# Kernel tuning notes

Measured on AMD Instinct MI355X. Metric: run time of the kernel, lower is better.

The kernel has to match this reference:

```python
import jax, jax.numpy as jnp
import numpy as np
import math

DIM = 2048
NUM_HEADS = 16
NUM_KV_HEADS = 4
HEAD_DIM = DIM // NUM_HEADS  # 128
KV_DIM = DIM * NUM_KV_HEADS // NUM_HEADS  # 512
B, T = 4, 2048


def setup_inputs() -> dict:
    key = jax.random.key(0)
    ks = jax.random.split(key, 12)
    s = 0.02
    return {
        "x": jax.random.normal(ks[0], (B, T, DIM), dtype=jnp.float32),
        "cos": jax.random.uniform(ks[1], (T, HEAD_DIM // 2), dtype=jnp.float32),
        "sin": jax.random.uniform(ks[2], (T, HEAD_DIM // 2), dtype=jnp.float32),
        "Wq": jax.random.normal(ks[3], (DIM, DIM), dtype=jnp.float32) * s,
        "bq": jnp.zeros((DIM,), dtype=jnp.float32),
        "Wk": jax.random.normal(ks[4], (DIM, KV_DIM), dtype=jnp.float32) * s,
        "bk": jnp.zeros((KV_DIM,), dtype=jnp.float32),
        "Wv": jax.random.normal(ks[5], (DIM, KV_DIM), dtype=jnp.float32) * s,
        "bv": jnp.zeros((KV_DIM,), dtype=jnp.float32),
        "Wo": jax.random.normal(ks[6], (DIM, DIM), dtype=jnp.float32) * s,
        "bo": jnp.zeros((DIM,), dtype=jnp.float32),
    }


def _rope(t, cos, sin):
    # t: [B, H, T, D]; cos/sin: [T, D/2] broadcast over (B, H)
    t1, t2 = t[..., ::2], t[..., 1::2]
    return jnp.concatenate([t1 * cos - t2 * sin, t1 * sin + t2 * cos], axis=-1)


def reference(x, cos, sin, Wq, bq, Wk, bk, Wv, bv, Wo, bo):
    Bx, Tx, C = x.shape
    q = (x @ Wq + bq).reshape(Bx, Tx, NUM_HEADS, HEAD_DIM).transpose(0, 2, 1, 3)
    k = (x @ Wk + bk).reshape(Bx, Tx, NUM_KV_HEADS, HEAD_DIM).transpose(0, 2, 1, 3)
    v = (x @ Wv + bv).reshape(Bx, Tx, NUM_KV_HEADS, HEAD_DIM).transpose(0, 2, 1, 3)
    rep = NUM_HEADS // NUM_KV_HEADS
    k = jnp.repeat(k, rep, axis=1)
    v = jnp.repeat(v, rep, axis=1)
    q = _rope(q, cos, sin)
    k = _rope(k, cos, sin)
    scores = jnp.einsum("bhqd,bhkd->bhqk", q, k) / math.sqrt(HEAD_DIM)
    attn = jax.nn.softmax(scores, axis=-1)
    out = jnp.einsum("bhqk,bhkd->bhqd", attn, v)
    out = out.transpose(0, 2, 1, 3).reshape(Bx, Tx, C)
    return out @ Wo + bo
```

## Files before the change

kernel.cpp:

```cpp
#include <hip/hip_runtime.h>

typedef unsigned short u16;
using bf16x8 = __attribute__((ext_vector_type(8))) short;
using u16x8  = __attribute__((ext_vector_type(8))) unsigned short;
using f32x4  = __attribute__((ext_vector_type(4))) float;
using u32x2  = __attribute__((ext_vector_type(2))) unsigned int;

__device__ __forceinline__ u16 f2bf(float f) {
  unsigned u = __float_as_uint(f);
  u += 0x7FFFu + ((u >> 16) & 1u);
  return (u16)(u >> 16);
}

__device__ __forceinline__ unsigned cvt_pk_bf16(float lo, float hi) {
  unsigned r;
  asm("v_cvt_pk_bf16_f32 %0, %1, %2" : "=v"(r) : "v"(lo), "v"(hi));
  return r;
}

__device__ __forceinline__ void gload_lds16(const void* g, void* l) {
  __builtin_amdgcn_global_load_lds(
      (const __attribute__((address_space(1))) unsigned int*)g,
      (__attribute__((address_space(3))) unsigned int*)l, 16, 0, 0);
}

__global__ __launch_bounds__(256) void k_cvt(const float* __restrict__ src,
                                             u16* __restrict__ dst) {
  size_t i = (size_t)blockIdx.x * 256 + threadIdx.x;
  const float4* s4 = (const float4*)src;
  float4 a = s4[i * 2], b = s4[i * 2 + 1];
  u16x8 r;
  r[0] = f2bf(a.x); r[1] = f2bf(a.y); r[2] = f2bf(a.z); r[3] = f2bf(a.w);
  r[4] = f2bf(b.x); r[5] = f2bf(b.y); r[6] = f2bf(b.z); r[7] = f2bf(b.w);
  *(u16x8*)(dst + i * 8) = r;
}

__global__ void k_transpose_cvt(const float* __restrict__ src, u16* __restrict__ dst,
                                int R, int C) {
  __shared__ float tile[32][33];
  int bx = blockIdx.x * 32, by = blockIdx.y * 32;
  int tx = threadIdx.x, ty = threadIdx.y;
#pragma unroll
  for (int j = 0; j < 4; ++j)
    tile[ty + j * 8][tx] = src[(size_t)(by + ty + j * 8) * C + bx + tx];
  __syncthreads();
#pragma unroll
  for (int j = 0; j < 4; ++j)
    dst[(size_t)(bx + ty + j * 8) * R + by + tx] = f2bf(tile[tx][ty + j * 8]);
}

__device__ __forceinline__ void gemm_core128(const u16* __restrict__ A,
                                             const u16* __restrict__ Bt, int K,
                                             int m0, int n0, u16* As, u16* Bs,
                                             f32x4 acc[4][4]) {
  const int tid  = threadIdx.x;
  const int lane = tid & 63;
  const int w    = tid >> 6;
  const int wr   = (w >> 1) * 64;
  const int wc   = (w & 1) * 64;
  const int srow = (w << 3) + (lane >> 3);
  const int lm   = lane & 15;
  const int lg   = lane >> 4;

  for (int kt = 0; kt < K; kt += 64) {
#pragma unroll
    for (int i = 0; i < 4; ++i) {
      int r  = (i << 5) + srow;
      int cc = (lane & 7) ^ (r & 7);
      gload_lds16(A  + (size_t)(m0 + r) * K + kt + (cc << 3), As + ((i * 4 + w) << 9));
      gload_lds16(Bt + (size_t)(n0 + r) * K + kt + (cc << 3), Bs + ((i * 4 + w) << 9));
    }
    __syncthreads();
#pragma unroll
    for (int kk = 0; kk < 2; ++kk) {
      bf16x8 af[4], bfr[4];
#pragma unroll
      for (int m = 0; m < 4; ++m) {
        const int row = wr + m * 16 + lm;
        af[m] = *(const bf16x8*)(As + row * 64 + ((((kk << 2) + lg) ^ (row & 7)) << 3));
      }
#pragma unroll
      for (int n = 0; n < 4; ++n) {
        const int row = wc + n * 16 + lm;
        bfr[n] = *(const bf16x8*)(Bs + row * 64 + ((((kk << 2) + lg) ^ (row & 7)) << 3));
      }
#pragma unroll
      for (int m = 0; m < 4; ++m)
#pragma unroll
        for (int n = 0; n < 4; ++n)
          acc[m][n] = __builtin_amdgcn_mfma_f32_16x16x32_bf16(af[m], bfr[n], acc[m][n], 0, 0, 0);
    }
    __syncthreads();
  }
}

__global__ __launch_bounds__(256, 2) void k_qkv(
    const u16* __restrict__ xb, const u16* __restrict__ wT,
    const float* __restrict__ bq, const float* __restrict__ bk, const float* __restrict__ bv,
    const float* __restrict__ cosb, const float* __restrict__ sinb,
    u16* __restrict__ qbuf, u16* __restrict__ kbuf, u16* __restrict__ vbufT) {
  __shared__ u16 As[128 * 64], Bs[128 * 64];
  const int mt = blockIdx.x, nt = blockIdx.y;
  f32x4 acc[4][4];
#pragma unroll
  for (int m = 0; m < 4; ++m)
#pragma unroll
    for (int n = 0; n < 4; ++n) { f32x4 z = {0.f, 0.f, 0.f, 0.f}; acc[m][n] = z; }
  gemm_core128(xb, wT, 2048, mt * 128, nt * 128, As, Bs, acc);

  const int lane = threadIdx.x & 63, w = threadIdx.x >> 6;
  const int row0 = mt * 128 + (w >> 1) * 64 + ((lane >> 4) << 2);
  const int col0 = nt * 128 + (w & 1) * 64 + (lane & 15);
  const float qscale = 0.12751744f;

#pragma unroll
  for (int m = 0; m < 4; ++m) {
#pragma unroll
    for (int n = 0; n < 4; ++n) {
      const int gc = col0 + n * 16;
#pragma unroll
      for (int i = 0; i < 4; ++i) {
        const int gr = row0 + m * 16 + i;
        const int b = gr >> 11, t = gr & 2047;
        float v = acc[m][n][i];
        if (nt < 16) {
          int h = gc >> 7, d = gc & 127;
          float val = v + bq[gc];
          float part = __shfl_xor(val, 1);
          int ir = d >> 1;
          float c = cosb[t * 64 + ir], s = sinb[t * 64 + ir];
          float outv; int dd;
          if (d & 1) { outv = part * s + val * c; dd = ir + 64; }
          else       { outv = val * c - part * s; dd = ir; }
          qbuf[(((size_t)(b * 16 + h) * 2048 + t) << 7) + dd] = f2bf(outv * qscale);
        } else if (nt < 20) {
          int g2 = gc - 2048;
          int kvh = g2 >> 7, d = g2 & 127;
          float val = v + bk[g2];
          float part = __shfl_xor(val, 1);
          int ir = d >> 1;
          float c = cosb[t * 64 + ir], s = sinb[t * 64 + ir];
          float outv; int dd;
          if (d & 1) { outv = part * s + val * c; dd = ir + 64; }
          else       { outv = val * c - part * s; dd = ir; }
          kbuf[(((size_t)(b * 4 + kvh) * 2048 + t) << 7) + dd] = f2bf(outv);
        } else {
          int g2 = gc - 2560;
          int kvh = g2 >> 7, d = g2 & 127;
          float val = v + bv[g2];
          vbufT[((size_t)((b * 4 + kvh) * 128 + d)) * 2048 + t] = f2bf(val);
        }
      }
    }
  }
}

__global__ __launch_bounds__(256, 2) void k_attn(const u16* __restrict__ qbuf,
                                                 const u16* __restrict__ kbuf,
                                                 const u16* __restrict__ vbufT,
                                                 u16* __restrict__ ob) {
  __shared__ u16 Ks[2][64 * 128];
  __shared__ u16 Vs[2][128 * 64];
  __shared__ u16 Ps[128 * 64];

  const int f = blockIdx.x;
  const int x = f & 7, mm = f >> 3;
  const int g = x * 2 + (mm >> 6);
  const int mem = mm & 63;
  const int b = g >> 2, kvh = g & 3;
  const int h = kvh * 4 + (mem >> 4);
  const int qt = mem & 15;

  const int tid = threadIdx.x, lane = tid & 63, w = tid >> 6;
  const int lm = lane & 15, lg = lane >> 4;

  const u16* qb = qbuf + ((size_t)((b * 16 + h) * 2048 + qt * 128)) * 128;
  const u16* kb = kbuf + ((size_t)(b * 4 + kvh) * 2048) * 128;
  const u16* vb = vbufT + ((size_t)(b * 4 + kvh) * 128) * 2048;

  bf16x8 qf[2][4];
#pragma unroll
  for (int st = 0; st < 2; ++st)
#pragma unroll
    for (int dc = 0; dc < 4; ++dc)
      qf[st][dc] = *(const bf16x8*)(qb + (size_t)(w * 32 + st * 16 + lm) * 128 + dc * 32 + (lg << 3));

  f32x4 o[2][8];
#pragma unroll
  for (int st = 0; st < 2; ++st)
#pragma unroll
    for (int dn = 0; dn < 8; ++dn) { f32x4 z = {0.f, 0.f, 0.f, 0.f}; o[st][dn] = z; }
  float lsum[2] = {0.f, 0.f};

  auto stage = [&](int buf, int kt) {
#pragma unroll
    for (int j = 0; j < 4; ++j) {
      int s  = w * 4 + j;
      int cK = s * 64 + lane;
      int rK = cK >> 4, ccK = cK & 15;
      gload_lds16(kb + (size_t)(kt + rK) * 128 + ((ccK ^ (rK & 7)) << 3), &Ks[buf][s << 9]);
      int dV = s * 8 + (lane >> 3), ccV = lane & 7;
      gload_lds16(vb + (size_t)dV * 2048 + kt + ((ccV ^ (dV & 7)) << 3), &Vs[buf][s << 9]);
    }
  };

  stage(0, 0);
  int cur = 0;
  for (int t = 0; t < 32; ++t) {
    const int kt = t << 6;
    if (t < 31) {
      stage(cur ^ 1, kt + 64);
      asm volatile("s_waitcnt vmcnt(8)" ::: "memory");
    } else {
      asm volatile("s_waitcnt vmcnt(0)" ::: "memory");
    }
    __builtin_amdgcn_s_barrier();
    __builtin_amdgcn_sched_barrier(0);
    const u16* KsC = Ks[cur];
    const u16* VsC = Vs[cur];

#pragma unroll
    for (int kg = 0; kg < 4; ++kg) {
      const int krow = kg * 16 + lm;
      bf16x8 kf[4];
#pragma unroll
      for (int dc = 0; dc < 4; ++dc)
        kf[dc] = *(const bf16x8*)(KsC + krow * 128 + (((dc * 4 + lg) ^ (krow & 7)) << 3));
      f32x4 s0 = {0.f, 0.f, 0.f, 0.f}, s1 = {0.f, 0.f, 0.f, 0.f};
      __builtin_amdgcn_s_setprio(1);
#pragma unroll
      for (int dc = 0; dc < 4; ++dc) {
        s0 = __builtin_amdgcn_mfma_f32_16x16x32_bf16(kf[dc], qf[0][dc], s0, 0, 0, 0);
        s1 = __builtin_amdgcn_mfma_f32_16x16x32_bf16(kf[dc], qf[1][dc], s1, 0, 0, 0);
      }
      __builtin_amdgcn_s_setprio(0);
#pragma unroll
      for (int st = 0; st < 2; ++st) {
        f32x4 sv = st ? s1 : s0;
        float p0 = __builtin_amdgcn_exp2f(sv[0]);
        float p1 = __builtin_amdgcn_exp2f(sv[1]);
        float p2 = __builtin_amdgcn_exp2f(sv[2]);
        float p3 = __builtin_amdgcn_exp2f(sv[3]);
        lsum[st] += (p0 + p1) + (p2 + p3);
        u32x2 pk;
        pk[0] = cvt_pk_bf16(p0, p1);
        pk[1] = cvt_pk_bf16(p2, p3);
        const int q = w * 32 + st * 16 + lm;
        const int chunk = kg * 2 + (lg >> 1);
        u16* dst = Ps + q * 64 + ((chunk ^ (q & 7)) << 3) + ((lg & 1) << 2);
        *reinterpret_cast<u32x2*>(dst) = pk;
      }
    }

#pragma unroll
    for (int kstep = 0; kstep < 2; ++kstep) {
      bf16x8 pf[2];
#pragma unroll
      for (int st = 0; st < 2; ++st) {
        const int q = w * 32 + st * 16 + lm;
        pf[st] = *(const bf16x8*)(Ps + q * 64 + (((kstep * 4 + lg) ^ (q & 7)) << 3));
      }
      __builtin_amdgcn_s_setprio(1);
#pragma unroll
      for (int dn = 0; dn < 8; ++dn) {
        const int d = dn * 16 + lm;
        bf16x8 vf = *(const bf16x8*)(VsC + d * 64 + (((kstep * 4 + lg) ^ (d & 7)) << 3));
        o[0][dn] = __builtin_amdgcn_mfma_f32_16x16x32_bf16(pf[0], vf, o[0][dn], 0, 0, 0);
        o[1][dn] = __builtin_amdgcn_mfma_f32_16x16x32_bf16(pf[1], vf, o[1][dn], 0, 0, 0);
      }
      __builtin_amdgcn_s_setprio(0);
    }
    __builtin_amdgcn_sched_barrier(0);
    __builtin_amdgcn_s_barrier();
    cur ^= 1;
  }

#pragma unroll
  for (int st = 0; st < 2; ++st) {
    float L = lsum[st];
    L += __shfl_xor(L, 16);
    L += __shfl_xor(L, 32);
#pragma unroll
    for (int i = 0; i < 4; ++i) {
      float inv = 1.0f / __shfl(L, lg * 4 + i);
      int t = qt * 128 + w * 32 + st * 16 + lg * 4 + i;
#pragma unroll
      for (int dn = 0; dn < 8; ++dn) {
        int d = dn * 16 + lm;
        ob[((size_t)(b * 2048 + t)) * 2048 + h * 128 + d] = f2bf(o[st][dn][i] * inv);
      }
    }
  }
}

__global__ __launch_bounds__(256, 2) void k_oproj(const u16* __restrict__ ab,
                                                  const u16* __restrict__ woT,
                                                  const float* __restrict__ bo,
                                                  float* __restrict__ out) {
  __shared__ u16 As[128 * 64], Bs[128 * 64];
  const int mt = blockIdx.x, nt = blockIdx.y;
  f32x4 acc[4][4];
#pragma unroll
  for (int m = 0; m < 4; ++m)
#pragma unroll
    for (int n = 0; n < 4; ++n) { f32x4 z = {0.f, 0.f, 0.f, 0.f}; acc[m][n] = z; }
  gemm_core128(ab, woT, 2048, mt * 128, nt * 128, As, Bs, acc);

  const int lane = threadIdx.x & 63, w = threadIdx.x >> 6;
  const int row0 = mt * 128 + (w >> 1) * 64 + ((lane >> 4) << 2);
  const int col0 = nt * 128 + (w & 1) * 64 + (lane & 15);
#pragma unroll
  for (int m = 0; m < 4; ++m)
#pragma unroll
    for (int n = 0; n < 4; ++n) {
      const int gc = col0 + n * 16;
      const float bias = bo[gc];
#pragma unroll
      for (int i = 0; i < 4; ++i) {
        const int gr = row0 + m * 16 + i;
        out[(size_t)gr * 2048 + gc] = acc[m][n][i] + bias;
      }
    }
}

extern "C" void kernel_launch(void* const* d_in, const int* in_sizes, int n_in,
                              void* d_out, int out_size, void* d_ws, size_t ws_size,
                              hipStream_t stream) {
  const float* x    = (const float*)d_in[0];
  const float* cosb = (const float*)d_in[1];
  const float* sinb = (const float*)d_in[2];
  const float* Wq   = (const float*)d_in[3];
  const float* bq   = (const float*)d_in[4];
  const float* Wk   = (const float*)d_in[5];
  const float* bk   = (const float*)d_in[6];
  const float* Wv   = (const float*)d_in[7];
  const float* bv   = (const float*)d_in[8];
  const float* Wo   = (const float*)d_in[9];
  const float* bo   = (const float*)d_in[10];
  float* out = (float*)d_out;

  u16* ws    = (u16*)d_ws;
  u16* xb    = ws;
  u16* wqkvT = xb    + (size_t)8192 * 2048;
  u16* woT   = wqkvT + (size_t)3072 * 2048;
  u16* qbuf  = woT   + (size_t)2048 * 2048;
  u16* kbuf  = qbuf  + (size_t)8192 * 2048;
  u16* vbufT = kbuf  + (size_t)8192 * 512;
  u16* attn  = xb;

  k_cvt<<<8192, 256, 0, stream>>>(x, xb);
  dim3 tb(32, 8);
  k_transpose_cvt<<<dim3(64, 64), tb, 0, stream>>>(Wq, wqkvT, 2048, 2048);
  k_transpose_cvt<<<dim3(16, 64), tb, 0, stream>>>(Wk, wqkvT + (size_t)2048 * 2048, 2048, 512);
  k_transpose_cvt<<<dim3(16, 64), tb, 0, stream>>>(Wv, wqkvT + (size_t)2560 * 2048, 2048, 512);
  k_transpose_cvt<<<dim3(64, 64), tb, 0, stream>>>(Wo, woT, 2048, 2048);

  k_qkv<<<dim3(64, 24), 256, 0, stream>>>(xb, wqkvT, bq, bk, bv, cosb, sinb, qbuf, kbuf, vbufT);
  k_attn<<<1024, 256, 0, stream>>>(qbuf, kbuf, vbufT, attn);
  k_oproj<<<dim3(64, 16), 256, 0, stream>>>(attn, woT, bo, out);
}
```

Baseline: 374.1 us.

## Use 32x32x16 MFMA in attention and keep P in registers via permlane swap

Rewrites the attention inner loop to use 32x32x16 bf16 MFMAs instead of 16x16x32. The S^T output layout is rearranged with v_permlane32_swap so the exponentiated probabilities feed the PV MFMA directly as A operands. This removes the LDS round trip through the Ps buffer and reduces MFMA instruction count and LDS traffic. In exchange it needs larger accumulator register tiles, which may raise register pressure and hurt occupancy, and it relies on exact lane-layout correctness.

Result: no change. 368.5 us (-1.5%).

```diff
diff --git a/kernel.cpp b/kernel.cpp
--- a/kernel.cpp
+++ b/kernel.cpp
@@ -4,7 +4,8 @@
 using bf16x8 = __attribute__((ext_vector_type(8))) short;
 using u16x8  = __attribute__((ext_vector_type(8))) unsigned short;
 using f32x4  = __attribute__((ext_vector_type(4))) float;
-using u32x2  = __attribute__((ext_vector_type(2))) unsigned int;
+using f32x16 = __attribute__((ext_vector_type(16))) float;
+using u32x4  = __attribute__((ext_vector_type(4))) unsigned int;
 
 __device__ __forceinline__ u16 f2bf(float f) {
   unsigned u = __float_as_uint(f);
@@ -16,6 +17,10 @@
   unsigned r;
   asm("v_cvt_pk_bf16_f32 %0, %1, %2" : "=v"(r) : "v"(lo), "v"(hi));
   return r;
+}
+
+__device__ __forceinline__ void permswap(unsigned& a, unsigned& b) {
+  asm volatile("v_permlane32_swap_b32 %0, %1" : "+v"(a), "+v"(b));
 }
 
 __device__ __forceinline__ void gload_lds16(const void* g, void* l) {
@@ -161,7 +166,6 @@
                                                  u16* __restrict__ ob) {
   __shared__ u16 Ks[2][64 * 128];
   __shared__ u16 Vs[2][128 * 64];
-  __shared__ u16 Ps[128 * 64];
 
   const int f = blockIdx.x;
   const int x = f & 7, mm = f >> 3;
@@ -172,25 +176,24 @@
   const int qt = mem & 15;
 
   const int tid = threadIdx.x, lane = tid & 63, w = tid >> 6;
-  const int lm = lane & 15, lg = lane >> 4;
+  const int l31 = lane & 31, hi = lane >> 5;
 
   const u16* qb = qbuf + ((size_t)((b * 16 + h) * 2048 + qt * 128)) * 128;
   const u16* kb = kbuf + ((size_t)(b * 4 + kvh) * 2048) * 128;
   const u16* vb = vbufT + ((size_t)(b * 4 + kvh) * 128) * 2048;
 
-  bf16x8 qf[2][4];
-#pragma unroll
-  for (int st = 0; st < 2; ++st)
-#pragma unroll
-    for (int dc = 0; dc < 4; ++dc)
-      qf[st][dc] = *(const bf16x8*)(qb + (size_t)(w * 32 + st * 16 + lm) * 128 + dc * 32 + (lg << 3));
-
-  f32x4 o[2][8];
-#pragma unroll
-  for (int st = 0; st < 2; ++st)
-#pragma unroll
-    for (int dn = 0; dn < 8; ++dn) { f32x4 z = {0.f, 0.f, 0.f, 0.f}; o[st][dn] = z; }
-  float lsum[2] = {0.f, 0.f};
+  const int q = w * 32 + l31;
+  bf16x8 qfr[8];
+#pragma unroll
+  for (int kc = 0; kc < 8; ++kc)
+    qfr[kc] = *(const bf16x8*)(qb + (size_t)q * 128 + kc * 16 + hi * 8);
+
+  f32x16 o[4];
+#pragma unroll
+  for (int dt = 0; dt < 4; ++dt)
+#pragma unroll
+    for (int r = 0; r < 16; ++r) o[dt][r] = 0.f;
+  float lsum = 0.f;
 
   auto stage = [&](int buf, int kt) {
 #pragma unroll
@@ -205,90 +208,83 @@
   };
 
   stage(0, 0);
-  int cur = 0;
   for (int t = 0; t < 32; ++t) {
-    const int kt = t << 6;
     if (t < 31) {
-      stage(cur ^ 1, kt + 64);
+      stage((t + 1) & 1, (t + 1) << 6);
       asm volatile("s_waitcnt vmcnt(8)" ::: "memory");
     } else {
       asm volatile("s_waitcnt vmcnt(0)" ::: "memory");
     }
     __builtin_amdgcn_s_barrier();
     __builtin_amdgcn_sched_barrier(0);
-    const u16* KsC = Ks[cur];
-    const u16* VsC = Vs[cur];
-
-#pragma unroll
-    for (int kg = 0; kg < 4; ++kg) {
-      const int krow = kg * 16 + lm;
-      bf16x8 kf[4];
-#pragma unroll
-      for (int dc = 0; dc < 4; ++dc)
-        kf[dc] = *(const bf16x8*)(KsC + krow * 128 + (((dc * 4 + lg) ^ (krow & 7)) << 3));
-      f32x4 s0 = {0.f, 0.f, 0.f, 0.f}, s1 = {0.f, 0.f, 0.f, 0.f};
+    const u16* KsC = Ks[t & 1];
+    const u16* VsC = Vs[t & 1];
+
+    u32x4 pa[4];
+
+#pragma unroll
+    for (int kb2 = 0; kb2 < 2; ++kb2) {
+      const int key = kb2 * 32 + l31;
+      bf16x8 kf[8];
+#pragma unroll
+      for (int kc = 0; kc < 8; ++kc)
+        kf[kc] = *(const bf16x8*)(KsC + key * 128 + (((kc * 2 + hi) ^ (key & 7)) << 3));
+      f32x16 s;
+#pragma unroll
+      for (int r = 0; r < 16; ++r) s[r] = 0.f;
       __builtin_amdgcn_s_setprio(1);
 #pragma unroll
-      for (int dc = 0; dc < 4; ++dc) {
-        s0 = __builtin_amdgcn_mfma_f32_16x16x32_bf16(kf[dc], qf[0][dc], s0, 0, 0, 0);
-        s1 = __builtin_amdgcn_mfma_f32_16x16x32_bf16(kf[dc], qf[1][dc], s1, 0, 0, 0);
-      }
+      for (int kc = 0; kc < 8; ++kc)
+        s = __builtin_amdgcn_mfma_f32_32x32x16_bf16(kf[kc], qfr[kc], s, 0, 0, 0);
       __builtin_amdgcn_s_setprio(0);
-#pragma unroll
-      for (int st = 0; st < 2; ++st) {
-        f32x4 sv = st ? s1 : s0;
-        float p0 = __builtin_amdgcn_exp2f(sv[0]);
-        float p1 = __builtin_amdgcn_exp2f(sv[1]);
-        float p2 = __builtin_amdgcn_exp2f(sv[2]);
-        float p3 = __builtin_amdgcn_exp2f(sv[3]);
-        lsum[st] += (p0 + p1) + (p2 + p3);
-        u32x2 pk;
-        pk[0] = cvt_pk_bf16(p0, p1);
-        pk[1] = cvt_pk_bf16(p2, p3);
-        const int q = w * 32 + st * 16 + lm;
-        const int chunk = kg * 2 + (lg >> 1);
-        u16* dst = Ps + q * 64 + ((chunk ^ (q & 7)) << 3) + ((lg & 1) << 2);
-        *reinterpret_cast<u32x2*>(dst) = pk;
-      }
-    }
-
-#pragma unroll
-    for (int kstep = 0; kstep < 2; ++kstep) {
-      bf16x8 pf[2];
-#pragma unroll
-      for (int st = 0; st < 2; ++st) {
-        const int q = w * 32 + st * 16 + lm;
-        pf[st] = *(const bf16x8*)(Ps + q * 64 + (((kstep * 4 + lg) ^ (q & 7)) << 3));
-      }
-      __builtin_amdgcn_s_setprio(1);
-#pragma unroll
-      for (int dn = 0; dn < 8; ++dn) {
-        const int d = dn * 16 + lm;
-        bf16x8 vf = *(const bf16x8*)(VsC + d * 64 + (((kstep * 4 + lg) ^ (d & 7)) << 3));
-        o[0][dn] = __builtin_amdgcn_mfma_f32_16x16x32_bf16(pf[0], vf, o[0][dn], 0, 0, 0);
-        o[1][dn] = __builtin_amdgcn_mfma_f32_16x16x32_bf16(pf[1], vf, o[1][dn], 0, 0, 0);
-      }
-      __builtin_amdgcn_s_setprio(0);
-    }
+
+      unsigned c[8];
+#pragma unroll
+      for (int j = 0; j < 8; ++j) {
+        float pa_ = __builtin_amdgcn_exp2f(s[2 * j]);
+        float pb_ = __builtin_amdgcn_exp2f(s[2 * j + 1]);
+        lsum += pa_ + pb_;
+        c[j] = cvt_pk_bf16(pa_, pb_);
+      }
+      unsigned t0 = c[0], t1 = c[2]; permswap(t0, t1);
+      unsigned t2 = c[1], t3 = c[3]; permswap(t2, t3);
+      u32x4 f0; f0[0] = t0; f0[1] = t2; f0[2] = t1; f0[3] = t3;
+      pa[kb2 * 2] = f0;
+      unsigned t4 = c[4], t5 = c[6]; permswap(t4, t5);
+      unsigned t6 = c[5], t7 = c[7]; permswap(t6, t7);
+      u32x4 f1; f1[0] = t4; f1[1] = t6; f1[2] = t5; f1[3] = t7;
+      pa[kb2 * 2 + 1] = f1;
+    }
+
+    __builtin_amdgcn_s_setprio(1);
+#pragma unroll
+    for (int dt = 0; dt < 4; ++dt) {
+      const int d = dt * 32 + l31;
+#pragma unroll
+      for (int ks = 0; ks < 4; ++ks) {
+        bf16x8 vf = *(const bf16x8*)(VsC + d * 64 + (((ks * 2 + hi) ^ (d & 7)) << 3));
+        bf16x8 af = __builtin_bit_cast(bf16x8, pa[ks]);
+        o[dt] = __builtin_amdgcn_mfma_f32_32x32x16_bf16(af, vf, o[dt], 0, 0, 0);
+      }
+    }
+    __builtin_amdgcn_s_setprio(0);
     __builtin_amdgcn_sched_barrier(0);
     __builtin_amdgcn_s_barrier();
-    cur ^= 1;
   }
 
-#pragma unroll
-  for (int st = 0; st < 2; ++st) {
-    float L = lsum[st];
-    L += __shfl_xor(L, 16);
-    L += __shfl_xor(L, 32);
-#pragma unroll
-    for (int i = 0; i < 4; ++i) {
-      float inv = 1.0f / __shfl(L, lg * 4 + i);
-      int t = qt * 128 + w * 32 + st * 16 + lg * 4 + i;
-#pragma unroll
-      for (int dn = 0; dn < 8; ++dn) {
-        int d = dn * 16 + lm;
-        ob[((size_t)(b * 2048 + t)) * 2048 + h * 128 + d] = f2bf(o[st][dn][i] * inv);
-      }
+  float L = lsum + __shfl_xor(lsum, 32);
+  float invL = 1.0f / L;
+  float iv[16];
+#pragma unroll
+  for (int r = 0; r < 16; ++r)
+    iv[r] = __shfl(invL, (r & 3) + 8 * (r >> 2) + 4 * hi);
+#pragma unroll
+  for (int dt = 0; dt < 4; ++dt) {
+    const int d = dt * 32 + l31;
+#pragma unroll
+    for (int r = 0; r < 16; ++r) {
+      const int tq = qt * 128 + w * 32 + (r & 3) + 8 * (r >> 2) + 4 * hi;
+      ob[((size_t)(b * 2048 + tq)) * 2048 + h * 128 + d] = f2bf(o[dt][r] * iv[r]);
     }
   }
 }
```
